# Optimization experiments

Measured on AMD Instinct MI355X. Metric: run time of the kernel, lower is better.

## Reference

```python
import jax, jax.numpy as jnp
import numpy as np

B, S, D = 32, 256, 384
N_LAYERS, N_HEAD, D_HEAD, D_INNER, K = 6, 1, 64, 1536, 3
DP_FILT, N_MEL, N_EMBED, PAD_IDX = 256, 80, 41, 0
PACE, MEL_MAX, MAX_DUR = 0.0265, 400, 75.0
ATTN_SCALE = 1.0 / float(np.sqrt(D_HEAD))


def layer_norm(x, g, b, eps=1e-5):
    mu = x.mean(-1, keepdims=True)
    v = ((x - mu) ** 2).mean(-1, keepdims=True)
    return (x - mu) * jax.lax.rsqrt(v + eps) * g + b


def conv1d(x, w, b, pad):
    # x: [B,T,Cin], w: [Cout,Cin,K] (torch layout) -> [B,T,Cout]
    y = jax.lax.conv_general_dilated(x, jnp.transpose(w, (2, 1, 0)), (1,), [(pad, pad)],
                                     dimension_numbers=('NWC', 'WIO', 'NWC'))
    return y + b


def pos_embedding(T, d):
    inv = 1.0 / (10000.0 ** (jnp.arange(0, d, 2, dtype=jnp.float32) / d))
    s = jnp.arange(T, dtype=jnp.float32)[:, None] * inv[None, :]
    return jnp.concatenate([jnp.sin(s), jnp.cos(s)], axis=-1)  # [T,d]


def fft_stack(x, mask, params):
    # x: [B,T,D], mask: [B,T,1]; params: tuple of arrays stacked over layers
    key_ok = (mask[..., 0] > 0)[:, None, None, :]  # [B,1,1,T]

    def body(h, p):
        qkv_w, qkv_b, o_w, ln1g, ln1b, c1w, c1b, c2w, c2b, ln2g, ln2b = p
        Bv, T, _ = h.shape
        qkv = h @ qkv_w + qkv_b
        q, k, v = [t.reshape(Bv, T, N_HEAD, D_HEAD) for t in jnp.split(qkv, 3, axis=-1)]
        sc = jnp.einsum('bqhd,bkhd->bhqk', q, k) * ATTN_SCALE
        a = jax.nn.softmax(jnp.where(key_ok, sc, -1e9), axis=-1)
        vec = jnp.einsum('bhqk,bkhd->bqhd', a, v).reshape(Bv, T, N_HEAD * D_HEAD)
        h = layer_norm(h + vec @ o_w, ln1g, ln1b) * mask   # post-norm MHA, then TransformerLayer mask
        c = jax.nn.relu(conv1d(h, c1w, c1b, (K - 1) // 2))
        c = conv1d(c, c2w, c2b, (K - 1) // 2)
        h = layer_norm(h + c, ln2g, ln2b) * mask           # post-norm conv-FF
        return h, None

    h, _ = jax.lax.scan(body, x, params)
    return h


def reference(inputs, dur_tgt, emb,
              enc_qkv_w, enc_qkv_b, enc_o_w, enc_ln1_g, enc_ln1_b,
              enc_c1_w, enc_c1_b, enc_c2_w, enc_c2_b, enc_ln2_g, enc_ln2_b,
              dec_qkv_w, dec_qkv_b, dec_o_w, dec_ln1_g, dec_ln1_b,
              dec_c1_w, dec_c1_b, dec_c2_w, dec_c2_b, dec_ln2_g, dec_ln2_b,
              dp_c1_w, dp_c1_b, dp_ln1_g, dp_ln1_b, dp_c2_w, dp_c2_b, dp_ln2_g, dp_ln2_b,
              dp_fc_w, dp_fc_b, proj_w, proj_b):
    # ---- encoder FFT (embed_input=True) ----
    enc_mask = (inputs != PAD_IDX)[..., None].astype(jnp.float32)  # [B,S,1]
    x = emb[inputs] + pos_embedding(S, D)[None] * enc_mask
    enc_out = fft_stack(x, enc_mask, (enc_qkv_w, enc_qkv_b, enc_o_w, enc_ln1_g, enc_ln1_b,
                                      enc_c1_w, enc_c1_b, enc_c2_w, enc_c2_b, enc_ln2_g, enc_ln2_b))
    h = enc_out * enc_mask
    h = layer_norm(jax.nn.relu(conv1d(h, dp_c1_w, dp_c1_b, K // 2)), dp_ln1_g, dp_ln1_b)
    h = layer_norm(jax.nn.relu(conv1d(h, dp_c2_w, dp_c2_b, K // 2)), dp_ln2_g, dp_ln2_b)
    log_dur_pred = ((h @ dp_fc_w + dp_fc_b) * enc_mask)[..., 0]
    dur_pred = jnp.clip(jnp.exp(log_dur_pred) - 1.0, 0.0, MAX_DUR)
    # ---- regulate_len (pace hardcoded to 0.0265; use_gt_durations=True path) ----
    reps = jnp.round(jax.lax.stop_gradient(dur_tgt) / PACE).astype(jnp.int32)  # .long() in torch
    cum = jnp.cumsum(reps, axis=1)          # [B,S]
    total = cum[:, -1]                      # full (unclipped) decoder lengths
    pos = jnp.arange(MEL_MAX)
    # frame t of sample b comes from phoneme i with cum[i-1] <= t < cum[i]
    idx = jax.vmap(lambda c: jnp.searchsorted(c, pos, side='right'))(cum)  # [B,MEL_MAX]
    idx = jnp.clip(idx, 0, S - 1)
    enc_rep = jax.vmap(lambda e, i: e[i])(enc_out, idx)  # [B,MEL_MAX,D]
    dec_lens = jnp.minimum(total, MEL_MAX)
    dec_mask = (pos[None, :] < dec_lens[:, None])[..., None].astype(jnp.float32)
    enc_rep = jnp.where(dec_mask > 0, enc_rep, 40.0)  # pad_sequence padding_value=40.0
    # ---- decoder FFT (embed_input=False) ----
    y = enc_rep + pos_embedding(MEL_MAX, D)[None] * dec_mask
    dec_out = fft_stack(y, dec_mask, (dec_qkv_w, dec_qkv_b, dec_o_w, dec_ln1_g, dec_ln1_b,
                                      dec_c1_w, dec_c1_b, dec_c2_w, dec_c2_b, dec_ln2_g, dec_ln2_b))
    mel_out = dec_out @ proj_w + proj_b
    return (mel_out, dec_mask, dur_pred, log_dur_pred, dec_lens)


def setup_inputs() -> dict:
    key = jax.random.key(0)
    ks = jax.random.split(key, 16)
    w = lambda k, shape: jax.random.normal(k, shape, dtype=jnp.float32) * 0.02
    L, A = N_LAYERS, 3 * N_HEAD * D_HEAD
    inputs = jax.random.randint(ks[0], (B, S), 0, N_EMBED, dtype=jnp.int32)
    # durations ~ U(0, 0.06) seconds -> repeats in {0,1,2}, ragged total lengths around MEL_MAX
    dur_tgt = jax.random.uniform(ks[1], (B, S), dtype=jnp.float32) * 0.06
    emb = w(ks[2], (N_EMBED, D)).at[PAD_IDX].set(0.0)
    d = dict(inputs=inputs, dur_tgt=dur_tgt, emb=emb)
    for name, k0 in (('enc', 3), ('dec', 7)):
        d[name + '_qkv_w'] = w(ks[k0], (L, D, A)); d[name + '_qkv_b'] = jnp.zeros((L, A))
        d[name + '_o_w'] = w(ks[k0 + 1], (L, N_HEAD * D_HEAD, D))
        d[name + '_ln1_g'] = jnp.ones((L, D)); d[name + '_ln1_b'] = jnp.zeros((L, D))
        d[name + '_c1_w'] = w(ks[k0 + 2], (L, D_INNER, D, K)); d[name + '_c1_b'] = jnp.zeros((L, D_INNER))
        d[name + '_c2_w'] = w(ks[k0 + 3], (L, D, D_INNER, K)); d[name + '_c2_b'] = jnp.zeros((L, D))
        d[name + '_ln2_g'] = jnp.ones((L, D)); d[name + '_ln2_b'] = jnp.zeros((L, D))
    d['dp_c1_w'] = w(ks[11], (DP_FILT, D, K)); d['dp_c1_b'] = jnp.zeros((DP_FILT,))
    d['dp_ln1_g'] = jnp.ones((DP_FILT,)); d['dp_ln1_b'] = jnp.zeros((DP_FILT,))
    d['dp_c2_w'] = w(ks[12], (DP_FILT, DP_FILT, K)); d['dp_c2_b'] = jnp.zeros((DP_FILT,))
    d['dp_ln2_g'] = jnp.ones((DP_FILT,)); d['dp_ln2_b'] = jnp.zeros((DP_FILT,))
    d['dp_fc_w'] = w(ks[13], (DP_FILT, 1)); d['dp_fc_b'] = jnp.zeros((1,))
    d['proj_w'] = w(ks[14], (D, N_MEL)); d['proj_b'] = jnp.zeros((N_MEL,))
    return d
```

## Files before the change

### kernel.cpp

```cpp
#include <hip/hip_runtime.h>
#include <hip/hip_bf16.h>
#include <stdint.h>

typedef __attribute__((ext_vector_type(8))) short bf16x8;
typedef __attribute__((ext_vector_type(4))) float f32x4;
typedef __attribute__((ext_vector_type(4))) unsigned int u32x4;

static constexpr int BB = 32, SS = 256, DD = 384;
static constexpr int TDEC = 400;
static constexpr int NMELC = 80;

static constexpr size_t OFF_MEL    = 0;
static constexpr size_t OFF_DMASK  = (size_t)BB * TDEC * NMELC;
static constexpr size_t OFF_DUR    = OFF_DMASK + (size_t)BB * TDEC;
static constexpr size_t OFF_LOGDUR = OFF_DUR + (size_t)BB * SS;
static constexpr size_t OFF_DLEN   = OFF_LOGDUR + (size_t)BB * SS;

__device__ __forceinline__ void gld16(void* lds, const void* g) {
  __builtin_amdgcn_global_load_lds(
      (const __attribute__((address_space(1))) void*)g,
      (__attribute__((address_space(3))) void*)lds, 16, 0, 0);
}


__global__ __launch_bounds__(256)
void transpose_cvt(const float* __restrict__ src, __hip_bfloat16* __restrict__ dst,
                   int R, int C, int Cpad)
{
  __shared__ float tile[32][33];
  int l = blockIdx.z;
  src += (size_t)l * R * C;
  dst += (size_t)l * Cpad * R;
  int r0 = blockIdx.x * 32, c0 = blockIdx.y * 32;
  int tx = threadIdx.x, ty = threadIdx.y;
  for (int i = ty; i < 32; i += 8) {
    int c = c0 + tx;
    tile[i][tx] = (c < C) ? src[(size_t)(r0 + i) * C + c] : 0.f;
  }
  __syncthreads();
  for (int i = ty; i < 32; i += 8) {
    dst[(size_t)(c0 + i) * R + (r0 + tx)] = __float2bfloat16(tile[tx][i]);
  }
}

__global__ __launch_bounds__(256)
void conv_cvt(const float* __restrict__ src, __hip_bfloat16* __restrict__ dst,
              int Cout, int Cin, long long total)
{
  long long i = (long long)blockIdx.x * 256 + threadIdx.x;
  if (i >= total) return;
  int ci = (int)(i % Cin);
  long long t1 = i / Cin;
  int co = (int)(t1 % Cout);
  long long t2 = t1 / Cout;
  int tap = (int)(t2 % 3);
  int l = (int)(t2 / 3);
  dst[i] = __float2bfloat16(src[(((size_t)l * Cout + co) * Cin + ci) * 3 + tap]);
}


__global__ __launch_bounds__(256)
void pe_kernel(float* __restrict__ pe, int T)
{
  int i = blockIdx.x * 256 + threadIdx.x;
  if (i >= T * 192) return;
  int t = i / 192, j = i % 192;
  float inv = expf(-(float)j * (9.210340371976184f / 192.f));
  float s = (float)t * inv;
  pe[(size_t)t * 384 + j]       = sinf(s);
  pe[(size_t)t * 384 + 192 + j] = cosf(s);
}

__global__ __launch_bounds__(128)
void embed_kernel(const int* __restrict__ inputs, const float* __restrict__ emb,
                  const float* __restrict__ pe, float* __restrict__ maskf,
                  float* __restrict__ xf, __hip_bfloat16* __restrict__ xb)
{
  int blk = blockIdx.x; int b = blk / SS, t = blk % SS;
  int tok = inputs[b * SS + t];
  float mk = (tok != 0) ? 1.f : 0.f;
  if (threadIdx.x == 0) maskf[b * SS + t] = mk;
  size_t prow = ((size_t)b * (SS + 2) + 1 + t) * 384;
  size_t drow = ((size_t)b * SS + t) * 384;
  for (int c = threadIdx.x; c < 384; c += 128) {
    float v = emb[(size_t)tok * 384 + c] + pe[(size_t)t * 384 + c] * mk;
    xf[drow + c] = v;
    xb[prow + c] = __float2bfloat16(v);
  }
}

__global__ __launch_bounds__(256)
void zero_guards(__hip_bfloat16* __restrict__ buf, int T, int C)
{
  int b = blockIdx.x >> 1, which = blockIdx.x & 1;
  size_t row = ((size_t)b * (T + 2) + (which ? (T + 1) : 0)) * (size_t)C;
  for (int c = threadIdx.x; c < C; c += 256) buf[row + c] = __float2bfloat16(0.f);
}

template<int TM, int DEPTH, int NTAPS, int KV, bool RELU, bool OUTF32, bool CPAD>
__global__ __launch_bounds__(256)
void gemm_tn(const __hip_bfloat16* __restrict__ A,
             const __hip_bfloat16* __restrict__ Bw,
             const float* __restrict__ bias,
             void* __restrict__ Cout_,
             int N, int ldc, int T, int Npad)
{
  constexpr int KS = KV >> 5;
  constexpr int NSTEP = NTAPS * KS;
  constexpr int DEP = (DEPTH < NSTEP) ? DEPTH : NSTEP;
  constexpr int NBUF = DEP + 1;
  constexpr int ABYTES = TM * 64;
  constexpr int BUFB = ABYTES + 8192;
  constexpr int MI_N = (TM == 128) ? 4 : 2;
  constexpr int OPS = (TM == 128) ? 4 : 3;
  constexpr int SLAST = NSTEP - 1 - DEP;
  __shared__ __align__(16) char SH[NBUF * BUFB];

  const int tid = threadIdx.x;
  const int lane = tid & 63;
  const int w = tid >> 6;
  const int wm = w >> 1, wn = w & 1;

  const int GN = gridDim.y;
  const int NB = gridDim.x * GN;
  const int f = blockIdx.y * gridDim.x + blockIdx.x;
  const int qq = NB >> 3, rr8 = NB & 7;
  const int xcd = f & 7, pos = f >> 3;
  const int st = (xcd < rr8) ? xcd * (qq + 1) : rr8 * (qq + 1) + (xcd - rr8) * qq;
  const int L = st + pos;
  const int m0 = (L / GN) * TM;
  const int n0 = (L % GN) * 128;

  const int ar = tid >> 2;
  const int q = tid & 3;
  const int qsw = q ^ ((ar >> 1) & 3);
  const int g0 = m0 + ar, g1 = g0 + 64;
  const char* sA0 = (const char*)A + (((size_t)(g0 + 2 * (g0 / T) + 1 - NTAPS / 2)) * KV + qsw * 8) * 2;
  const char* sA1 = (const char*)A + (((size_t)(g1 + 2 * (g1 / T) + 1 - NTAPS / 2)) * KV + qsw * 8) * 2;
  const char* sB0 = (const char*)Bw + ((size_t)(n0 + ar) * KV + qsw * 8) * 2;
  const char* sB1 = (const char*)Bw + ((size_t)(n0 + ar + 64) * KV + qsw * 8) * 2;

  const int woff = ar * 64 + q * 16;
  int ks_s = 0;

  auto STAGE = [&](int buf) {
    char* base = SH + buf * BUFB;
    gld16(base + woff, sA0);
    if (TM == 128) gld16(base + 4096 + woff, sA1);
    gld16(base + ABYTES + woff, sB0);
    gld16(base + ABYTES + 4096 + woff, sB1);
  };
  auto ADV = [&]() {
    sA0 += 64; sA1 += 64; sB0 += 64; sB1 += 64;
    if (++ks_s == KS) {
      ks_s = 0;
      const size_t badj = ((size_t)Npad - 1) * KV * 2;
      sB0 += badj; sB1 += badj;
    }
  };

  f32x4 zero = {0.f, 0.f, 0.f, 0.f};
  f32x4 acc[MI_N][4];
#pragma unroll
  for (int i = 0; i < MI_N; i++)
#pragma unroll
    for (int j = 0; j < 4; j++) acc[i][j] = zero;

  const int rl = lane & 15;
  const int hi4 = lane >> 4;
  const int kb2 = (hi4 ^ ((rl >> 1) & 3)) * 16;

#pragma unroll
  for (int i = 0; i < DEP; ++i) { STAGE(i); ADV(); }
  if constexpr (DEP == NSTEP) {
    asm volatile("s_waitcnt vmcnt(0)" ::: "memory");
  } else {
    asm volatile("s_waitcnt vmcnt(%0)" :: "i"((DEP - 1) * OPS) : "memory");
  }
  __builtin_amdgcn_s_barrier();
  __builtin_amdgcn_sched_barrier(0);

  int cur = 0;
  for (int s = 0; s < NSTEP; ++s) {
    if (s + DEP < NSTEP) {
      int nb = cur + DEP; if (nb >= NBUF) nb -= NBUF;
      STAGE(nb); ADV();
    }
    const char* Ab = SH + cur * BUFB;
    const char* Bb = Ab + ABYTES;
    bf16x8 af[MI_N], bfr[4];
#pragma unroll
    for (int mi = 0; mi < MI_N; mi++)
      af[mi] = *(const bf16x8*)(Ab + (wm * (TM / 2) + mi * 16 + rl) * 64 + kb2);
#pragma unroll
    for (int ni = 0; ni < 4; ni++)
      bfr[ni] = *(const bf16x8*)(Bb + (wn * 64 + ni * 16 + rl) * 64 + kb2);
#pragma unroll
    for (int mi = 0; mi < MI_N; mi++)
#pragma unroll
      for (int ni = 0; ni < 4; ni++)
        acc[mi][ni] = __builtin_amdgcn_mfma_f32_16x16x32_bf16(af[mi], bfr[ni], acc[mi][ni], 0, 0, 0);
    if (s < SLAST) {
      asm volatile("s_waitcnt vmcnt(%0)" :: "i"(((DEP > 1 ? DEP : 2) - 1) * OPS) : "memory");
      __builtin_amdgcn_s_barrier();
      __builtin_amdgcn_sched_barrier(0);
    } else if (s == SLAST) {
      asm volatile("s_waitcnt vmcnt(0)" ::: "memory");
      __builtin_amdgcn_s_barrier();
      __builtin_amdgcn_sched_barrier(0);
    }
    cur = cur + 1; if (cur >= NBUF) cur -= NBUF;
  }

  const int rj = hi4 * 4;
  if (!OUTF32) {
    __syncthreads();
    ushort* S = (ushort*)SH;
#pragma unroll
    for (int mi = 0; mi < MI_N; mi++) {
#pragma unroll
      for (int ni = 0; ni < 4; ni++) {
        int lc = wn * 64 + ni * 16 + rl;
        float bv = bias ? bias[n0 + lc] : 0.f;
#pragma unroll
        for (int j = 0; j < 4; j++) {
          float v = acc[mi][ni][j] + bv;
          if (RELU) v = fmaxf(v, 0.f);
          __hip_bfloat16 hb = __float2bfloat16(v);
          S[(wm * (TM / 2) + mi * 16 + rj + j) * 128 + lc] = *(ushort*)&hb;
        }
      }
    }
    __syncthreads();
    const int tr = tid >> 4;
    const int tc = (tid & 15) * 8;
#pragma unroll
    for (int pass = 0; pass < TM / 16; ++pass) {
      int lr = pass * 16 + tr;
      int gcol = n0 + tc;
      if (gcol < N) {
        int r = m0 + lr;
        size_t orow = CPAD ? ((size_t)r + 2 * (r / T) + 1) : (size_t)r;
        *(u32x4*)((__hip_bfloat16*)Cout_ + orow * ldc + gcol) = *(const u32x4*)&S[lr * 128 + tc];
      }
    }
  } else {
#pragma unroll
    for (int mi = 0; mi < MI_N; mi++) {
#pragma unroll
      for (int ni = 0; ni < 4; ni++) {
        int col = n0 + wn * 64 + ni * 16 + rl;
        if (col < N) {
          float bv = bias ? bias[col] : 0.f;
#pragma unroll
          for (int j = 0; j < 4; j++) {
            int r = m0 + wm * (TM / 2) + mi * 16 + rj + j;
            float v = acc[mi][ni][j] + bv;
            if (RELU) v = fmaxf(v, 0.f);
            size_t orow = CPAD ? ((size_t)r + 2 * (r / T) + 1) : (size_t)r;
            ((float*)Cout_)[orow * ldc + col] = v;
          }
        }
      }
    }
  }
}

__global__ __launch_bounds__(256)
void fattn_kernel(const __hip_bfloat16* __restrict__ qkv, const float* __restrict__ maskf,
                  __hip_bfloat16* __restrict__ vec, int T, int NT)
{
  __shared__ __align__(16) ushort VT[64][456];
  __shared__ __align__(16) ushort Pl[4][16][72];
  __shared__ float MS[448];

  const int tid = threadIdx.x;
  const int b = blockIdx.y;
  const int TP = T + 2;
  const int KTOT = NT * 64;
  const char* bptr = (const char*)qkv + ((size_t)b * TP + 1) * 384;

  for (int k = tid; k < KTOT; k += 256)
    MS[k] = (k < T) ? ((maskf[b * T + k] > 0.f) ? 0.f : -1e9f) : -1e38f;
  for (int i = tid; i < KTOT * 8; i += 256) {
    int k = i >> 3, seg = i & 7;
    int kr = (k < T) ? k : T - 1;
    uint4 u = *(const uint4*)(bptr + (size_t)kr * 384 + 256 + seg * 16);
    const ushort* e = (const ushort*)&u;
#pragma unroll
    for (int j = 0; j < 8; ++j) VT[seg * 8 + j][k] = e[j];
  }
  __syncthreads();

  const int w = tid >> 6, lane = tid & 63;
  const int lo = lane & 15, hi = lane >> 4;
  const int q0 = blockIdx.x * 64 + w * 16;
  const int qc = min(q0 + lo, T - 1);

  bf16x8 afr[2];
#pragma unroll
  for (int ks = 0; ks < 2; ++ks)
    afr[ks] = *(const bf16x8*)(bptr + (size_t)qc * 384 + ks * 64 + hi * 16);

  f32x4 Oacc[4];
  f32x4 z = {0.f, 0.f, 0.f, 0.f};
#pragma unroll
  for (int df = 0; df < 4; ++df) Oacc[df] = z;
  float mrun[4], lrun[4];
#pragma unroll
  for (int j = 0; j < 4; ++j) { mrun[j] = -3e38f; lrun[j] = 0.f; }

  for (int kt = 0; kt < NT; ++kt) {
    const int kb = kt * 64;
    f32x4 S[4];
#pragma unroll
    for (int f = 0; f < 4; ++f) S[f] = z;
#pragma unroll
    for (int ks = 0; ks < 2; ++ks) {
#pragma unroll
      for (int f = 0; f < 4; ++f) {
        int krc = min(kb + f * 16 + lo, T - 1);
        bf16x8 bfr = *(const bf16x8*)(bptr + (size_t)krc * 384 + 128 + ks * 64 + hi * 16);
        S[f] = __builtin_amdgcn_mfma_f32_16x16x32_bf16(afr[ks], bfr, S[f], 0, 0, 0);
      }
    }
    float sv[4][4];
#pragma unroll
    for (int f = 0; f < 4; ++f) {
      float msel = MS[kb + f * 16 + lo];
#pragma unroll
      for (int j = 0; j < 4; ++j) {
        float x = S[f][j] * 0.125f;
        sv[f][j] = (msel == 0.f) ? x : msel;
      }
    }
    float scale[4];
#pragma unroll
    for (int j = 0; j < 4; ++j) {
      float m4 = fmaxf(fmaxf(sv[0][j], sv[1][j]), fmaxf(sv[2][j], sv[3][j]));
#pragma unroll
      for (int msk = 1; msk < 16; msk <<= 1) m4 = fmaxf(m4, __shfl_xor(m4, msk));
      float mnew = fmaxf(mrun[j], m4);
      scale[j] = __expf(mrun[j] - mnew);
      mrun[j] = mnew;
    }
    float pv[4][4], ps[4] = {0.f, 0.f, 0.f, 0.f};
#pragma unroll
    for (int f = 0; f < 4; ++f)
#pragma unroll
      for (int j = 0; j < 4; ++j) {
        float p = __expf(sv[f][j] - mrun[j]);
        pv[f][j] = p; ps[j] += p;
      }
#pragma unroll
    for (int j = 0; j < 4; ++j) {
#pragma unroll
      for (int msk = 1; msk < 16; msk <<= 1) ps[j] += __shfl_xor(ps[j], msk);
      lrun[j] = lrun[j] * scale[j] + ps[j];
#pragma unroll
      for (int df = 0; df < 4; ++df) Oacc[df][j] *= scale[j];
    }
#pragma unroll
    for (int f = 0; f < 4; ++f)
#pragma unroll
      for (int j = 0; j < 4; ++j) {
        __hip_bfloat16 hb = __float2bfloat16(pv[f][j]);
        Pl[w][hi * 4 + j][f * 16 + lo] = *(ushort*)&hb;
      }
#pragma unroll
    for (int ks = 0; ks < 2; ++ks) {
      bf16x8 pa = *(const bf16x8*)((const char*)&Pl[w][lo][0] + ks * 64 + hi * 16);
#pragma unroll
      for (int df = 0; df < 4; ++df) {
        bf16x8 vfr = *(const bf16x8*)((const char*)&VT[df * 16 + lo][0] + kb * 2 + ks * 64 + hi * 16);
        Oacc[df] = __builtin_amdgcn_mfma_f32_16x16x32_bf16(pa, vfr, Oacc[df], 0, 0, 0);
      }
    }
  }

  float inv[4];
#pragma unroll
  for (int j = 0; j < 4; ++j) inv[j] = 1.f / lrun[j];
#pragma unroll
  for (int df = 0; df < 4; ++df)
#pragma unroll
    for (int j = 0; j < 4; ++j) {
      int qq = q0 + hi * 4 + j;
      if (qq < T) {
        __hip_bfloat16 hb = __float2bfloat16(Oacc[df][j] * inv[j]);
        *(ushort*)((char*)vec + ((size_t)b * TP + 1 + qq) * 128 + (df * 16 + lo) * 2) = *(ushort*)&hb;
      }
    }
}

template<bool HASRES, bool HASMASK>
__global__ __launch_bounds__(128)
void ln_kernel(const __hip_bfloat16* __restrict__ xin, const float* __restrict__ resin,
               const float* __restrict__ g, const float* __restrict__ bb,
               const float* __restrict__ maskf,
               float* __restrict__ outf, __hip_bfloat16* __restrict__ outb,
               int C, int T)
{
  int blk = blockIdx.x; int b = blk / T, t = blk % T;
  size_t prow = ((size_t)b * (T + 2) + 1 + t) * C;
  size_t drow = ((size_t)b * T + t) * C;
  int tid = threadIdx.x;
  float vals[3];
  float s1 = 0.f, s2 = 0.f;
  int nv = 0;
  for (int c = tid; c < C; c += 128) {
    float v = __bfloat162float(xin[prow + c]);
    if (HASRES) v += resin[drow + c];
    vals[nv++] = v; s1 += v; s2 += v * v;
  }
  __shared__ float r1[128], r2[128];
  r1[tid] = s1; r2[tid] = s2;
  __syncthreads();
  for (int s = 64; s > 0; s >>= 1) {
    if (tid < s) { r1[tid] += r1[tid + s]; r2[tid] += r2[tid + s]; }
    __syncthreads();
  }
  float mu = r1[0] / C;
  float var = r2[0] / C - mu * mu;
  float rstd = rsqrtf(fmaxf(var, 0.f) + 1e-5f);
  float mk = HASMASK ? maskf[b * T + t] : 1.f;
  nv = 0;
  for (int c = tid; c < C; c += 128) {
    float o = ((vals[nv++] - mu) * rstd * g[c] + bb[c]) * mk;
    if (outf) outf[drow + c] = o;
    outb[prow + c] = __float2bfloat16(o);
  }
}

__global__ __launch_bounds__(64)
void dpfc_kernel(const __hip_bfloat16* __restrict__ dp2, const float* __restrict__ fcw,
                 const float* __restrict__ fcb, const float* __restrict__ maskf,
                 float* __restrict__ logdur, float* __restrict__ durpred)
{
  int blk = blockIdx.x; int b = blk / SS, t = blk % SS;
  size_t prow = ((size_t)b * (SS + 2) + 1 + t) * 256;
  int lane = threadIdx.x;
  float a = 0.f;
  for (int c = lane; c < 256; c += 64) a += __bfloat162float(dp2[prow + c]) * fcw[c];
  for (int o = 32; o > 0; o >>= 1) a += __shfl_down(a, o);
  if (lane == 0) {
    float ld = (a + fcb[0]) * maskf[b * SS + t];
    logdur[b * SS + t] = ld;
    durpred[b * SS + t] = fminf(fmaxf(expf(ld) - 1.f, 0.f), 75.f);
  }
}

__global__ __launch_bounds__(512)
void regulator_kernel(const float* __restrict__ dur, float* __restrict__ dmaskf,
                      int* __restrict__ idxbuf, float* __restrict__ out_dmask,
                      float* __restrict__ out_dlen)
{
  int b = blockIdx.x, tid = threadIdx.x;
  __shared__ int cum[256];
  __shared__ int len_s;
  if (tid < 256) cum[tid] = (int)rintf(dur[b * 256 + tid] / 0.0265f);
  __syncthreads();
  if (tid == 0) {
    int acc = 0;
    for (int i = 0; i < 256; i++) { acc += cum[i]; cum[i] = acc; }
    int len = acc < 400 ? acc : 400;
    len_s = len;
    out_dlen[b] = (float)len;
  }
  __syncthreads();
  if (tid < 400) {
    int p = tid;
    int lo = 0, hi = 256;
    while (lo < hi) { int mid = (lo + hi) >> 1; if (cum[mid] <= p) lo = mid + 1; else hi = mid; }
    int idx = lo < 255 ? lo : 255;
    idxbuf[b * 400 + p] = idx;
    float mk = (p < len_s) ? 1.f : 0.f;
    dmaskf[b * 400 + p] = mk;
    out_dmask[b * 400 + p] = mk;
  }
}

__global__ __launch_bounds__(128)
void build_y_kernel(const float* __restrict__ encf, const int* __restrict__ idxbuf,
                    const float* __restrict__ dmaskf, const float* __restrict__ pe,
                    float* __restrict__ yf, __hip_bfloat16* __restrict__ yb)
{
  int blk = blockIdx.x; int b = blk / 400, p = blk % 400;
  float mk = dmaskf[b * 400 + p];
  int idx = idxbuf[b * 400 + p];
  size_t orowp = ((size_t)b * 402 + 1 + p) * 384;
  size_t orowd = ((size_t)b * 400 + p) * 384;
  size_t srow = ((size_t)b * 256 + idx) * 384;
  for (int c = threadIdx.x; c < 384; c += 128) {
    float v = (mk > 0.f) ? (encf[srow + c] + pe[(size_t)p * 384 + c]) : 40.f;
    yf[orowd + c] = v;
    yb[orowp + c] = __float2bfloat16(v);
  }
}

extern "C" void kernel_launch(void* const* d_in, const int* in_sizes, int n_in,
                              void* d_out, int out_size, void* d_ws, size_t ws_size,
                              hipStream_t stream)
{
  (void)in_sizes; (void)n_in; (void)out_size; (void)ws_size;
  float* outF = (float*)d_out;

  const int*   inputs  = (const int*)d_in[0];
  const float* dur_tgt = (const float*)d_in[1];
  const float* emb     = (const float*)d_in[2];
  const float* e_qkv_w = (const float*)d_in[3];
  const float* e_qkv_b = (const float*)d_in[4];
  const float* e_o_w   = (const float*)d_in[5];
  const float* e_ln1g  = (const float*)d_in[6];
  const float* e_ln1b  = (const float*)d_in[7];
  const float* e_c1w   = (const float*)d_in[8];
  const float* e_c1b   = (const float*)d_in[9];
  const float* e_c2w   = (const float*)d_in[10];
  const float* e_c2b   = (const float*)d_in[11];
  const float* e_ln2g  = (const float*)d_in[12];
  const float* e_ln2b  = (const float*)d_in[13];
  const float* dc_qkv_w = (const float*)d_in[14];
  const float* dc_qkv_b = (const float*)d_in[15];
  const float* dc_o_w   = (const float*)d_in[16];
  const float* dc_ln1g  = (const float*)d_in[17];
  const float* dc_ln1b  = (const float*)d_in[18];
  const float* dc_c1w   = (const float*)d_in[19];
  const float* dc_c1b   = (const float*)d_in[20];
  const float* dc_c2w   = (const float*)d_in[21];
  const float* dc_c2b   = (const float*)d_in[22];
  const float* dc_ln2g  = (const float*)d_in[23];
  const float* dc_ln2b  = (const float*)d_in[24];
  const float* dp_c1w = (const float*)d_in[25];
  const float* dp_c1b = (const float*)d_in[26];
  const float* dp_ln1g = (const float*)d_in[27];
  const float* dp_ln1b = (const float*)d_in[28];
  const float* dp_c2w = (const float*)d_in[29];
  const float* dp_c2b = (const float*)d_in[30];
  const float* dp_ln2g = (const float*)d_in[31];
  const float* dp_ln2b = (const float*)d_in[32];
  const float* dp_fcw = (const float*)d_in[33];
  const float* dp_fcb = (const float*)d_in[34];
  const float* proj_w = (const float*)d_in[35];
  const float* proj_b = (const float*)d_in[36];

  char* ws = (char*)d_ws;
  size_t off = 0;
  auto alloc = [&](size_t bytes) -> char* {
    char* p = ws + off;
    off += (bytes + 255) & ~(size_t)255;
    return p;
  };

  __hip_bfloat16* qkvwt_e = (__hip_bfloat16*)alloc((size_t)6 * 256 * 384 * 2);
  __hip_bfloat16* qkvwt_d = (__hip_bfloat16*)alloc((size_t)6 * 256 * 384 * 2);
  __hip_bfloat16* owt_e   = (__hip_bfloat16*)alloc((size_t)6 * 384 * 64 * 2);
  __hip_bfloat16* owt_d   = (__hip_bfloat16*)alloc((size_t)6 * 384 * 64 * 2);
  __hip_bfloat16* c1wt_e  = (__hip_bfloat16*)alloc((size_t)6 * 3 * 1536 * 384 * 2);
  __hip_bfloat16* c1wt_d  = (__hip_bfloat16*)alloc((size_t)6 * 3 * 1536 * 384 * 2);
  __hip_bfloat16* c2wt_e  = (__hip_bfloat16*)alloc((size_t)6 * 3 * 384 * 1536 * 2);
  __hip_bfloat16* c2wt_d  = (__hip_bfloat16*)alloc((size_t)6 * 3 * 384 * 1536 * 2);
  __hip_bfloat16* dpc1wt  = (__hip_bfloat16*)alloc((size_t)3 * 256 * 384 * 2);
  __hip_bfloat16* dpc2wt  = (__hip_bfloat16*)alloc((size_t)3 * 256 * 256 * 2);
  __hip_bfloat16* projwt  = (__hip_bfloat16*)alloc((size_t)128 * 384 * 2);
  float* pe_e   = (float*)alloc((size_t)256 * 384 * 4);
  float* pe_d   = (float*)alloc((size_t)400 * 384 * 4);
  float* maskf_e = (float*)alloc((size_t)32 * 256 * 4);
  float* maskf_d = (float*)alloc((size_t)32 * 400 * 4);
  int*   idxbuf  = (int*)alloc((size_t)32 * 400 * 4);
  __hip_bfloat16* h_enc_bf = (__hip_bfloat16*)alloc((size_t)32 * 258 * 384 * 2);
  float*          h_enc_f  = (float*)alloc((size_t)32 * 256 * 384 * 4);
  __hip_bfloat16* h_dec_bf = (__hip_bfloat16*)alloc((size_t)32 * 402 * 384 * 2);
  float*          h_dec_f  = (float*)alloc((size_t)32 * 400 * 384 * 4);
  __hip_bfloat16* qkvbuf = (__hip_bfloat16*)alloc((size_t)32 * 402 * 192 * 2);
  __hip_bfloat16* vecbuf = (__hip_bfloat16*)alloc((size_t)32 * 402 * 64 * 2);
  __hip_bfloat16* tmp384 = (__hip_bfloat16*)alloc((size_t)32 * 402 * 384 * 2);
  __hip_bfloat16* cbuf   = (__hip_bfloat16*)alloc((size_t)32 * 402 * 1536 * 2);
  __hip_bfloat16* dp1b   = (__hip_bfloat16*)alloc((size_t)32 * 258 * 256 * 2);
  __hip_bfloat16* dp2b   = (__hip_bfloat16*)alloc((size_t)32 * 258 * 256 * 2);

  transpose_cvt<<<dim3(12, 8, 6), dim3(32, 8), 0, stream>>>(e_qkv_w, qkvwt_e, 384, 192, 256);
  transpose_cvt<<<dim3(12, 8, 6), dim3(32, 8), 0, stream>>>(dc_qkv_w, qkvwt_d, 384, 192, 256);
  transpose_cvt<<<dim3(2, 12, 6), dim3(32, 8), 0, stream>>>(e_o_w, owt_e, 64, 384, 384);
  transpose_cvt<<<dim3(2, 12, 6), dim3(32, 8), 0, stream>>>(dc_o_w, owt_d, 64, 384, 384);
  transpose_cvt<<<dim3(12, 4, 1), dim3(32, 8), 0, stream>>>(proj_w, projwt, 384, 80, 128);
  {
    long long tot = 6LL * 3 * 1536 * 384;
    int blocks = (int)((tot + 255) / 256);
    conv_cvt<<<blocks, 256, 0, stream>>>(e_c1w, c1wt_e, 1536, 384, tot);
    conv_cvt<<<blocks, 256, 0, stream>>>(dc_c1w, c1wt_d, 1536, 384, tot);
    conv_cvt<<<blocks, 256, 0, stream>>>(e_c2w, c2wt_e, 384, 1536, tot);
    conv_cvt<<<blocks, 256, 0, stream>>>(dc_c2w, c2wt_d, 384, 1536, tot);
  }
  { long long tot = 3LL * 256 * 384; conv_cvt<<<(int)((tot + 255) / 256), 256, 0, stream>>>(dp_c1w, dpc1wt, 256, 384, tot); }
  { long long tot = 3LL * 256 * 256; conv_cvt<<<(int)((tot + 255) / 256), 256, 0, stream>>>(dp_c2w, dpc2wt, 256, 256, tot); }

  pe_kernel<<<(256 * 192 + 255) / 256, 256, 0, stream>>>(pe_e, 256);
  pe_kernel<<<(400 * 192 + 255) / 256, 256, 0, stream>>>(pe_d, 400);

  embed_kernel<<<32 * 256, 128, 0, stream>>>(inputs, emb, pe_e, maskf_e, h_enc_f, h_enc_bf);
  zero_guards<<<64, 256, 0, stream>>>(h_enc_bf, 256, 384);
  zero_guards<<<64, 256, 0, stream>>>(cbuf, 256, 1536);

  for (int l = 0; l < 6; ++l) {
    gemm_tn<64, 4, 1, 384, false, false, true><<<dim3(128, 2), 256, 0, stream>>>(
        h_enc_bf, qkvwt_e + (size_t)l * 256 * 384, e_qkv_b + l * 192, qkvbuf,
        192, 192, 256, 256);
    fattn_kernel<<<dim3(4, 32), 256, 0, stream>>>(qkvbuf, maskf_e, vecbuf, 256, 4);
    gemm_tn<64, 4, 1, 64, false, false, true><<<dim3(128, 3), 256, 0, stream>>>(
        vecbuf, owt_e + (size_t)l * 384 * 64, nullptr, tmp384,
        384, 384, 256, 384);
    ln_kernel<true, true><<<32 * 256, 128, 0, stream>>>(
        tmp384, h_enc_f, e_ln1g + l * 384, e_ln1b + l * 384, maskf_e, h_enc_f, h_enc_bf, 384, 256);
    gemm_tn<128, 2, 3, 384, true, false, true><<<dim3(64, 12), 256, 0, stream>>>(
        h_enc_bf, c1wt_e + (size_t)l * 3 * 1536 * 384, e_c1b + l * 1536, cbuf,
        1536, 1536, 256, 1536);
    gemm_tn<64, 4, 3, 1536, false, false, true><<<dim3(128, 3), 256, 0, stream>>>(
        cbuf, c2wt_e + (size_t)l * 3 * 384 * 1536, e_c2b + l * 384, tmp384,
        384, 384, 256, 384);
    ln_kernel<true, true><<<32 * 256, 128, 0, stream>>>(
        tmp384, h_enc_f, e_ln2g + l * 384, e_ln2b + l * 384, maskf_e, h_enc_f, h_enc_bf, 384, 256);
  }

  zero_guards<<<64, 256, 0, stream>>>(dp1b, 256, 256);
  gemm_tn<64, 4, 3, 384, true, false, true><<<dim3(128, 2), 256, 0, stream>>>(
      h_enc_bf, dpc1wt, dp_c1b, dp1b, 256, 256, 256, 256);
  ln_kernel<false, false><<<32 * 256, 128, 0, stream>>>(
      dp1b, nullptr, dp_ln1g, dp_ln1b, nullptr, nullptr, dp1b, 256, 256);
  gemm_tn<64, 4, 3, 256, true, false, true><<<dim3(128, 2), 256, 0, stream>>>(
      dp1b, dpc2wt, dp_c2b, dp2b, 256, 256, 256, 256);
  ln_kernel<false, false><<<32 * 256, 128, 0, stream>>>(
      dp2b, nullptr, dp_ln2g, dp_ln2b, nullptr, nullptr, dp2b, 256, 256);
  dpfc_kernel<<<32 * 256, 64, 0, stream>>>(
      dp2b, dp_fcw, dp_fcb, maskf_e, outF + OFF_LOGDUR, outF + OFF_DUR);

  regulator_kernel<<<32, 512, 0, stream>>>(dur_tgt, maskf_d, idxbuf,
                                           outF + OFF_DMASK, outF + OFF_DLEN);
  zero_guards<<<64, 256, 0, stream>>>(h_dec_bf, 400, 384);
  zero_guards<<<64, 256, 0, stream>>>(cbuf, 400, 1536);
  build_y_kernel<<<32 * 400, 128, 0, stream>>>(h_enc_f, idxbuf, maskf_d, pe_d, h_dec_f, h_dec_bf);

  for (int l = 0; l < 6; ++l) {
    gemm_tn<64, 4, 1, 384, false, false, true><<<dim3(200, 2), 256, 0, stream>>>(
        h_dec_bf, qkvwt_d + (size_t)l * 256 * 384, dc_qkv_b + l * 192, qkvbuf,
        192, 192, 400, 256);
    fattn_kernel<<<dim3(7, 32), 256, 0, stream>>>(qkvbuf, maskf_d, vecbuf, 400, 7);
    gemm_tn<64, 4, 1, 64, false, false, true><<<dim3(200, 3), 256, 0, stream>>>(
        vecbuf, owt_d + (size_t)l * 384 * 64, nullptr, tmp384,
        384, 384, 400, 384);
    ln_kernel<true, true><<<32 * 400, 128, 0, stream>>>(
        tmp384, h_dec_f, dc_ln1g + l * 384, dc_ln1b + l * 384, maskf_d, h_dec_f, h_dec_bf, 384, 400);
    gemm_tn<128, 2, 3, 384, true, false, true><<<dim3(100, 12), 256, 0, stream>>>(
        h_dec_bf, c1wt_d + (size_t)l * 3 * 1536 * 384, dc_c1b + l * 1536, cbuf,
        1536, 1536, 400, 1536);
    gemm_tn<64, 4, 3, 1536, false, false, true><<<dim3(200, 3), 256, 0, stream>>>(
        cbuf, c2wt_d + (size_t)l * 3 * 384 * 1536, dc_c2b + l * 384, tmp384,
        384, 384, 400, 384);
    ln_kernel<true, true><<<32 * 400, 128, 0, stream>>>(
        tmp384, h_dec_f, dc_ln2g + l * 384, dc_ln2b + l * 384, maskf_d, h_dec_f, h_dec_bf, 384, 400);
  }

  gemm_tn<64, 4, 1, 384, false, true, false><<<dim3(200, 1), 256, 0, stream>>>(
      h_dec_bf, projwt, proj_b, outF + OFF_MEL, 80, 80, 400, 128);
}
```

Baseline: 2.380 ms.

## Drop fp32 residual stream, use warp-per-row layernorm, shallower GEMM pipeline

```diff
diff --git a/kernel.cpp b/kernel.cpp
--- a/kernel.cpp
+++ b/kernel.cpp
@@ -74,17 +74,15 @@
 __global__ __launch_bounds__(128)
 void embed_kernel(const int* __restrict__ inputs, const float* __restrict__ emb,
                   const float* __restrict__ pe, float* __restrict__ maskf,
-                  float* __restrict__ xf, __hip_bfloat16* __restrict__ xb)
+                  __hip_bfloat16* __restrict__ xb)
 {
   int blk = blockIdx.x; int b = blk / SS, t = blk % SS;
   int tok = inputs[b * SS + t];
   float mk = (tok != 0) ? 1.f : 0.f;
   if (threadIdx.x == 0) maskf[b * SS + t] = mk;
   size_t prow = ((size_t)b * (SS + 2) + 1 + t) * 384;
-  size_t drow = ((size_t)b * SS + t) * 384;
   for (int c = threadIdx.x; c < 384; c += 128) {
     float v = emb[(size_t)tok * 384 + c] + pe[(size_t)t * 384 + c] * mk;
-    xf[drow + c] = v;
     xb[prow + c] = __float2bfloat16(v);
   }
 }
@@ -113,7 +111,6 @@
   constexpr int BUFB = ABYTES + 8192;
   constexpr int MI_N = (TM == 128) ? 4 : 2;
   constexpr int OPS = (TM == 128) ? 4 : 3;
-  constexpr int SLAST = NSTEP - 1 - DEP;
   __shared__ __align__(16) char SH[NBUF * BUFB];
 
   const int tid = threadIdx.x;
@@ -200,12 +197,12 @@
 #pragma unroll
       for (int ni = 0; ni < 4; ni++)
         acc[mi][ni] = __builtin_amdgcn_mfma_f32_16x16x32_bf16(af[mi], bfr[ni], acc[mi][ni], 0, 0, 0);
-    if (s < SLAST) {
-      asm volatile("s_waitcnt vmcnt(%0)" :: "i"(((DEP > 1 ? DEP : 2) - 1) * OPS) : "memory");
-      __builtin_amdgcn_s_barrier();
-      __builtin_amdgcn_sched_barrier(0);
-    } else if (s == SLAST) {
-      asm volatile("s_waitcnt vmcnt(0)" ::: "memory");
+    if (s + 1 < NSTEP) {
+      if (s + DEP < NSTEP) {
+        asm volatile("s_waitcnt vmcnt(%0)" :: "i"((DEP - 1) * OPS) : "memory");
+      } else {
+        asm volatile("s_waitcnt vmcnt(0)" ::: "memory");
+      }
       __builtin_amdgcn_s_barrier();
       __builtin_amdgcn_sched_barrier(0);
     }
@@ -393,42 +390,51 @@
     }
 }
 
-template<bool HASRES, bool HASMASK>
-__global__ __launch_bounds__(128)
-void ln_kernel(const __hip_bfloat16* __restrict__ xin, const float* __restrict__ resin,
+template<int C, bool HASRES, bool HASMASK>
+__global__ __launch_bounds__(256)
+void ln_kernel(const __hip_bfloat16* __restrict__ xin, const __hip_bfloat16* __restrict__ resin,
                const float* __restrict__ g, const float* __restrict__ bb,
                const float* __restrict__ maskf,
-               float* __restrict__ outf, __hip_bfloat16* __restrict__ outb,
-               int C, int T)
-{
-  int blk = blockIdx.x; int b = blk / T, t = blk % T;
-  size_t prow = ((size_t)b * (T + 2) + 1 + t) * C;
-  size_t drow = ((size_t)b * T + t) * C;
-  int tid = threadIdx.x;
-  float vals[3];
+               __hip_bfloat16* __restrict__ outb, int T)
+{
+  constexpr int NU = C / 128;
+  const int row = blockIdx.x * 4 + (threadIdx.x >> 6);
+  const int lane = threadIdx.x & 63;
+  const int b = row / T, t = row - b * T;
+  const size_t prow = ((size_t)b * (T + 2) + 1 + t) * C;
+  const uint* xu = (const uint*)(xin + prow);
+  const uint* ru = (const uint*)(resin + prow);
+  float v[2 * NU];
   float s1 = 0.f, s2 = 0.f;
-  int nv = 0;
-  for (int c = tid; c < C; c += 128) {
-    float v = __bfloat162float(xin[prow + c]);
-    if (HASRES) v += resin[drow + c];
-    vals[nv++] = v; s1 += v; s2 += v * v;
-  }
-  __shared__ float r1[128], r2[128];
-  r1[tid] = s1; r2[tid] = s2;
-  __syncthreads();
-  for (int s = 64; s > 0; s >>= 1) {
-    if (tid < s) { r1[tid] += r1[tid + s]; r2[tid] += r2[tid + s]; }
-    __syncthreads();
-  }
-  float mu = r1[0] / C;
-  float var = r2[0] / C - mu * mu;
+#pragma unroll
+  for (int k = 0; k < NU; ++k) {
+    uint ux = xu[lane + 64 * k];
+    uint xl = ux << 16, xh = ux & 0xffff0000u;
+    float lo = *(float*)&xl, hi = *(float*)&xh;
+    if (HASRES) {
+      uint ur = ru[lane + 64 * k];
+      uint rl2 = ur << 16, rh = ur & 0xffff0000u;
+      lo += *(float*)&rl2; hi += *(float*)&rh;
+    }
+    v[2 * k] = lo; v[2 * k + 1] = hi;
+    s1 += lo + hi; s2 += lo * lo + hi * hi;
+  }
+#pragma unroll
+  for (int o = 32; o > 0; o >>= 1) { s1 += __shfl_xor(s1, o); s2 += __shfl_xor(s2, o); }
+  float mu = s1 / C;
+  float var = s2 / C - mu * mu;
   float rstd = rsqrtf(fmaxf(var, 0.f) + 1e-5f);
-  float mk = HASMASK ? maskf[b * T + t] : 1.f;
-  nv = 0;
-  for (int c = tid; c < C; c += 128) {
-    float o = ((vals[nv++] - mu) * rstd * g[c] + bb[c]) * mk;
-    if (outf) outf[drow + c] = o;
-    outb[prow + c] = __float2bfloat16(o);
+  float mk = HASMASK ? maskf[row] : 1.f;
+  uint* ou = (uint*)(outb + prow);
+#pragma unroll
+  for (int k = 0; k < NU; ++k) {
+    int c = (lane + 64 * k) * 2;
+    float2 gv = *(const float2*)(g + c);
+    float2 bv = *(const float2*)(bb + c);
+    float lo = ((v[2 * k]     - mu) * rstd * gv.x + bv.x) * mk;
+    float hi = ((v[2 * k + 1] - mu) * rstd * gv.y + bv.y) * mk;
+    __hip_bfloat16 hl = __float2bfloat16(lo), hh = __float2bfloat16(hi);
+    ou[lane + 64 * k] = (uint)(*(ushort*)&hl) | ((uint)(*(ushort*)&hh) << 16);
   }
 }
 
@@ -481,19 +487,17 @@
 }
 
 __global__ __launch_bounds__(128)
-void build_y_kernel(const float* __restrict__ encf, const int* __restrict__ idxbuf,
+void build_y_kernel(const __hip_bfloat16* __restrict__ encb, const int* __restrict__ idxbuf,
                     const float* __restrict__ dmaskf, const float* __restrict__ pe,
-                    float* __restrict__ yf, __hip_bfloat16* __restrict__ yb)
+                    __hip_bfloat16* __restrict__ yb)
 {
   int blk = blockIdx.x; int b = blk / 400, p = blk % 400;
   float mk = dmaskf[b * 400 + p];
   int idx = idxbuf[b * 400 + p];
   size_t orowp = ((size_t)b * 402 + 1 + p) * 384;
-  size_t orowd = ((size_t)b * 400 + p) * 384;
-  size_t srow = ((size_t)b * 256 + idx) * 384;
+  size_t srow = ((size_t)b * 258 + 1 + idx) * 384;
   for (int c = threadIdx.x; c < 384; c += 128) {
-    float v = (mk > 0.f) ? (encf[srow + c] + pe[(size_t)p * 384 + c]) : 40.f;
-    yf[orowd + c] = v;
+    float v = (mk > 0.f) ? (__bfloat162float(encb[srow + c]) + pe[(size_t)p * 384 + c]) : 40.f;
     yb[orowp + c] = __float2bfloat16(v);
   }
 }
@@ -568,9 +572,7 @@
   float* maskf_d = (float*)alloc((size_t)32 * 400 * 4);
   int*   idxbuf  = (int*)alloc((size_t)32 * 400 * 4);
   __hip_bfloat16* h_enc_bf = (__hip_bfloat16*)alloc((size_t)32 * 258 * 384 * 2);
-  float*          h_enc_f  = (float*)alloc((size_t)32 * 256 * 384 * 4);
   __hip_bfloat16* h_dec_bf = (__hip_bfloat16*)alloc((size_t)32 * 402 * 384 * 2);
-  float*          h_dec_f  = (float*)alloc((size_t)32 * 400 * 384 * 4);
   __hip_bfloat16* qkvbuf = (__hip_bfloat16*)alloc((size_t)32 * 402 * 192 * 2);
   __hip_bfloat16* vecbuf = (__hip_bfloat16*)alloc((size_t)32 * 402 * 64 * 2);
   __hip_bfloat16* tmp384 = (__hip_bfloat16*)alloc((size_t)32 * 402 * 384 * 2);
@@ -597,39 +599,39 @@
   pe_kernel<<<(256 * 192 + 255) / 256, 256, 0, stream>>>(pe_e, 256);
   pe_kernel<<<(400 * 192 + 255) / 256, 256, 0, stream>>>(pe_d, 400);
 
-  embed_kernel<<<32 * 256, 128, 0, stream>>>(inputs, emb, pe_e, maskf_e, h_enc_f, h_enc_bf);
+  embed_kernel<<<32 * 256, 128, 0, stream>>>(inputs, emb, pe_e, maskf_e, h_enc_bf);
   zero_guards<<<64, 256, 0, stream>>>(h_enc_bf, 256, 384);
   zero_guards<<<64, 256, 0, stream>>>(cbuf, 256, 1536);
 
   for (int l = 0; l < 6; ++l) {
-    gemm_tn<64, 4, 1, 384, false, false, true><<<dim3(128, 2), 256, 0, stream>>>(
+    gemm_tn<64, 2, 1, 384, false, false, true><<<dim3(128, 2), 256, 0, stream>>>(
         h_enc_bf, qkvwt_e + (size_t)l * 256 * 384, e_qkv_b + l * 192, qkvbuf,
         192, 192, 256, 256);
     fattn_kernel<<<dim3(4, 32), 256, 0, stream>>>(qkvbuf, maskf_e, vecbuf, 256, 4);
-    gemm_tn<64, 4, 1, 64, false, false, true><<<dim3(128, 3), 256, 0, stream>>>(
+    gemm_tn<64, 2, 1, 64, false, false, true><<<dim3(128, 3), 256, 0, stream>>>(
         vecbuf, owt_e + (size_t)l * 384 * 64, nullptr, tmp384,
         384, 384, 256, 384);
-    ln_kernel<true, true><<<32 * 256, 128, 0, stream>>>(
-        tmp384, h_enc_f, e_ln1g + l * 384, e_ln1b + l * 384, maskf_e, h_enc_f, h_enc_bf, 384, 256);
+    ln_kernel<384, true, true><<<2048, 256, 0, stream>>>(
+        tmp384, h_enc_bf, e_ln1g + l * 384, e_ln1b + l * 384, maskf_e, h_enc_bf, 256);
     gemm_tn<128, 2, 3, 384, true, false, true><<<dim3(64, 12), 256, 0, stream>>>(
         h_enc_bf, c1wt_e + (size_t)l * 3 * 1536 * 384, e_c1b + l * 1536, cbuf,
         1536, 1536, 256, 1536);
-    gemm_tn<64, 4, 3, 1536, false, false, true><<<dim3(128, 3), 256, 0, stream>>>(
+    gemm_tn<64, 2, 3, 1536, false, false, true><<<dim3(128, 3), 256, 0, stream>>>(
         cbuf, c2wt_e + (size_t)l * 3 * 384 * 1536, e_c2b + l * 384, tmp384,
         384, 384, 256, 384);
-    ln_kernel<true, true><<<32 * 256, 128, 0, stream>>>(
-        tmp384, h_enc_f, e_ln2g + l * 384, e_ln2b + l * 384, maskf_e, h_enc_f, h_enc_bf, 384, 256);
+    ln_kernel<384, true, true><<<2048, 256, 0, stream>>>(
+        tmp384, h_enc_bf, e_ln2g + l * 384, e_ln2b + l * 384, maskf_e, h_enc_bf, 256);
   }
 
   zero_guards<<<64, 256, 0, stream>>>(dp1b, 256, 256);
-  gemm_tn<64, 4, 3, 384, true, false, true><<<dim3(128, 2), 256, 0, stream>>>(
+  gemm_tn<64, 2, 3, 384, true, false, true><<<dim3(128, 2), 256, 0, stream>>>(
       h_enc_bf, dpc1wt, dp_c1b, dp1b, 256, 256, 256, 256);
-  ln_kernel<false, false><<<32 * 256, 128, 0, stream>>>(
-      dp1b, nullptr, dp_ln1g, dp_ln1b, nullptr, nullptr, dp1b, 256, 256);
-  gemm_tn<64, 4, 3, 256, true, false, true><<<dim3(128, 2), 256, 0, stream>>>(
+  ln_kernel<256, false, false><<<2048, 256, 0, stream>>>(
+      dp1b, nullptr, dp_ln1g, dp_ln1b, nullptr, dp1b, 256);
+  gemm_tn<64, 2, 3, 256, true, false, true><<<dim3(128, 2), 256, 0, stream>>>(
       dp1b, dpc2wt, dp_c2b, dp2b, 256, 256, 256, 256);
-  ln_kernel<false, false><<<32 * 256, 128, 0, stream>>>(
-      dp2b, nullptr, dp_ln2g, dp_ln2b, nullptr, nullptr, dp2b, 256, 256);
+  ln_kernel<256, false, false><<<2048, 256, 0, stream>>>(
+      dp2b, nullptr, dp_ln2g, dp_ln2b, nullptr, dp2b, 256);
   dpfc_kernel<<<32 * 256, 64, 0, stream>>>(
       dp2b, dp_fcw, dp_fcb, maskf_e, outF + OFF_LOGDUR, outF + OFF_DUR);
 
@@ -637,28 +639,28 @@
                                            outF + OFF_DMASK, outF + OFF_DLEN);
   zero_guards<<<64, 256, 0, stream>>>(h_dec_bf, 400, 384);
   zero_guards<<<64, 256, 0, stream>>>(cbuf, 400, 1536);
-  build_y_kernel<<<32 * 400, 128, 0, stream>>>(h_enc_f, idxbuf, maskf_d, pe_d, h_dec_f, h_dec_bf);
+  build_y_kernel<<<32 * 400, 128, 0, stream>>>(h_enc_bf, idxbuf, maskf_d, pe_d, h_dec_bf);
 
   for (int l = 0; l < 6; ++l) {
-    gemm_tn<64, 4, 1, 384, false, false, true><<<dim3(200, 2), 256, 0, stream>>>(
+    gemm_tn<64, 2, 1, 384, false, false, true><<<dim3(200, 2), 256, 0, stream>>>(
         h_dec_bf, qkvwt_d + (size_t)l * 256 * 384, dc_qkv_b + l * 192, qkvbuf,
         192, 192, 400, 256);
     fattn_kernel<<<dim3(7, 32), 256, 0, stream>>>(qkvbuf, maskf_d, vecbuf, 400, 7);
-    gemm_tn<64, 4, 1, 64, false, false, true><<<dim3(200, 3), 256, 0, stream>>>(
+    gemm_tn<64, 2, 1, 64, false, false, true><<<dim3(200, 3), 256, 0, stream>>>(
         vecbuf, owt_d + (size_t)l * 384 * 64, nullptr, tmp384,
         384, 384, 400, 384);
-    ln_kernel<true, true><<<32 * 400, 128, 0, stream>>>(
-        tmp384, h_dec_f, dc_ln1g + l * 384, dc_ln1b + l * 384, maskf_d, h_dec_f, h_dec_bf, 384, 400);
+    ln_kernel<384, true, true><<<3200, 256, 0, stream>>>(
+        tmp384, h_dec_bf, dc_ln1g + l * 384, dc_ln1b + l * 384, maskf_d, h_dec_bf, 400);
     gemm_tn<128, 2, 3, 384, true, false, true><<<dim3(100, 12), 256, 0, stream>>>(
         h_dec_bf, c1wt_d + (size_t)l * 3 * 1536 * 384, dc_c1b + l * 1536, cbuf,
         1536, 1536, 400, 1536);
-    gemm_tn<64, 4, 3, 1536, false, false, true><<<dim3(200, 3), 256, 0, stream>>>(
+    gemm_tn<64, 2, 3, 1536, false, false, true><<<dim3(200, 3), 256, 0, stream>>>(
         cbuf, c2wt_d + (size_t)l * 3 * 384 * 1536, dc_c2b + l * 384, tmp384,
         384, 384, 400, 384);
-    ln_kernel<true, true><<<32 * 400, 128, 0, stream>>>(
-        tmp384, h_dec_f, dc_ln2g + l * 384, dc_ln2b + l * 384, maskf_d, h_dec_f, h_dec_bf, 384, 400);
-  }
-
-  gemm_tn<64, 4, 1, 384, false, true, false><<<dim3(200, 1), 256, 0, stream>>>(
+    ln_kernel<384, true, true><<<3200, 256, 0, stream>>>(
+        tmp384, h_dec_bf, dc_ln2g + l * 384, dc_ln2b + l * 384, maskf_d, h_dec_bf, 400);
+  }
+
+  gemm_tn<64, 2, 1, 384, false, true, false><<<dim3(200, 1), 256, 0, stream>>>(
       h_dec_bf, projwt, proj_b, outF + OFF_MEL, 80, 80, 400, 128);
 }
```

After: 2.166 ms. 1.1x faster.
